# Performance work log

Hardware: AMD Instinct MI355X
Metric: run time of the kernel (lower is better)

## Reference

```python
import jax, jax.numpy as jnp
import numpy as np

N_NODES = 50000
N_EDGES = 800000
HIDDEN = 128


def setup_inputs() -> dict:
    key = jax.random.key(0)
    k1, k2, k3, k4, k5, k6 = jax.random.split(key, 6)
    node_features = jax.random.normal(k1, (N_NODES, HIDDEN), dtype=jnp.float32)
    src = jax.random.randint(k2, (N_EDGES,), 0, N_NODES)
    tgt = jax.random.randint(k3, (N_EDGES,), 0, N_NODES)
    gcn_norm = jax.random.uniform(k4, (N_EDGES,), dtype=jnp.float32)
    scale = 1.0 / np.sqrt(HIDDEN)
    W1 = jax.random.normal(k5, (HIDDEN, HIDDEN), dtype=jnp.float32) * scale
    b1 = jnp.zeros((HIDDEN,), dtype=jnp.float32)
    W2 = jax.random.normal(k6, (HIDDEN, HIDDEN), dtype=jnp.float32) * scale
    b2 = jnp.zeros((HIDDEN,), dtype=jnp.float32)
    return {"node_features": node_features, "src": src, "tgt": tgt,
            "gcn_norm": gcn_norm, "W1": W1, "b1": b1, "W2": W2, "b2": b2}


def reference(node_features, src, tgt, gcn_norm, W1, b1, W2, b2):
    # broadcast source node states to edges: [E, H]
    edge_states = node_features[src]
    # edge Dense + activation, scaled by gcn normalization (dropout = identity at inference)
    messages = gcn_norm[:, None] * jax.nn.relu(edge_states @ W1 + b1)
    # scatter-sum messages to target nodes: [N, H]
    pooled = jax.ops.segment_sum(messages, tgt, num_segments=node_features.shape[0])
    # node Dense + activation, then residual add of target feature
    hidden = jax.nn.relu(pooled @ W2 + b2)
    return hidden + node_features
```

## Files before the change

### kernel.cpp

```cpp
#include <hip/hip_runtime.h>

#define H 128

typedef short short8 __attribute__((ext_vector_type(8)));
typedef float floatx4 __attribute__((ext_vector_type(4)));

__device__ __forceinline__ short f2bf(float f) {
  union { float f; unsigned u; } v; v.f = f;
  unsigned r = v.u + 0x7fffu + ((v.u >> 16) & 1u);
  return (short)(r >> 16);
}
__device__ __forceinline__ float bf2f(unsigned u16) {
  union { unsigned u; float f; } v; v.u = u16 << 16;
  return v.f;
}

__global__ __launch_bounds__(256) void pack_count(
    const float* __restrict__ W1, const float* __restrict__ W2,
    short* __restrict__ Bp1, short* __restrict__ Bp2,
    const int* __restrict__ tgt, int* __restrict__ counts,
    int* __restrict__ rank, int E) {
  if (blockIdx.x < 16) {
    const int t = blockIdx.x * 256 + threadIdx.x;
    const float* W = (t >> 11) ? W2 : W1;
    short* Bp = (t >> 11) ? Bp2 : Bp1;
    const int i = t & 2047;
    const int lane = i & 63, ks = (i >> 6) & 3, nt = i >> 8;
    const int n = nt * 16 + (lane & 15);
    const int k0 = ks * 32 + ((lane >> 4) << 3);
    short8 v;
#pragma unroll
    for (int j = 0; j < 8; j++) v[j] = f2bf(W[(k0 + j) * H + n]);
    *reinterpret_cast<short8*>(Bp + (size_t)i * 8) = v;
  } else {
    const int e = (blockIdx.x - 16) * 256 + threadIdx.x;
    if (e < E) rank[e] = atomicAdd(&counts[tgt[e]], 1);
  }
}

template <bool A_BF16, bool C_BF16, bool RESID>
__global__ __launch_bounds__(256) void gemm_mfma(
    const void* __restrict__ Av, const short* __restrict__ Bp,
    const float* __restrict__ bias, const float* __restrict__ R,
    void* __restrict__ Cv, int M) {
  __shared__ int4 bLds[2048];
  const int tid = threadIdx.x;
  {
    const int4* g = reinterpret_cast<const int4*>(Bp);
#pragma unroll
    for (int i = 0; i < 8; i++) bLds[tid + i * 256] = g[tid + i * 256];
  }
  __syncthreads();

  const int wv = tid >> 6;
  const int lane = tid & 63;
  const int m0 = blockIdx.x * 64 + wv * 16;

  floatx4 acc[8];
#pragma unroll
  for (int nt = 0; nt < 8; nt++) acc[nt] = (floatx4)0.f;

  const int arow = lane & 15;
  const int kb = (lane >> 4) << 3;
  const short8* bL = reinterpret_cast<const short8*>(bLds);

#pragma unroll
  for (int ks = 0; ks < 4; ks++) {
    short8 af;
    {
      int row = min(m0 + arow, M - 1);
      const size_t off = (size_t)row * H + (ks << 5) + kb;
      if (A_BF16) {
        af = *reinterpret_cast<const short8*>((const short*)Av + off);
      } else {
        const float* ap = (const float*)Av + off;
        floatx4 x0 = *reinterpret_cast<const floatx4*>(ap);
        floatx4 x1 = *reinterpret_cast<const floatx4*>(ap + 4);
        af[0] = f2bf(x0[0]); af[1] = f2bf(x0[1]);
        af[2] = f2bf(x0[2]); af[3] = f2bf(x0[3]);
        af[4] = f2bf(x1[0]); af[5] = f2bf(x1[1]);
        af[6] = f2bf(x1[2]); af[7] = f2bf(x1[3]);
      }
    }
#pragma unroll
    for (int nt = 0; nt < 8; nt++) {
      const short8 bf = bL[((nt << 2) | ks) * 64 + lane];
      acc[nt] = __builtin_amdgcn_mfma_f32_16x16x32_bf16(af, bf, acc[nt], 0, 0, 0);
    }
  }

  const int crow = (lane >> 4) << 2;
  const int ccol = lane & 15;
#pragma unroll
  for (int nt = 0; nt < 8; nt++) {
    const int col = (nt << 4) + ccol;
    const float bv = bias[col];
#pragma unroll
    for (int r = 0; r < 4; r++) {
      const int row = m0 + crow + r;
      if (row < M) {
        float v = fmaxf(acc[nt][r] + bv, 0.f);
        if (RESID) v += R[(size_t)row * H + col];
        if (C_BF16)
          ((short*)Cv)[(size_t)row * H + col] = f2bf(v);
        else
          ((float*)Cv)[(size_t)row * H + col] = v;
      }
    }
  }
}


__global__ __launch_bounds__(256) void scan_partial(
    const int* __restrict__ counts, int* __restrict__ blockSums, int N) {
  const int tid = threadIdx.x;
  const int base = blockIdx.x * 1024 + tid * 4;
  int4 v = make_int4(0, 0, 0, 0);
  if (base + 3 < N) {
    v = *reinterpret_cast<const int4*>(counts + base);
  } else if (base < N) {
    const int n = N - base;
    v.x = counts[base];
    if (n > 1) v.y = counts[base + 1];
    if (n > 2) v.z = counts[base + 2];
  }
  int s = v.x + v.y + v.z + v.w;
#pragma unroll
  for (int d = 1; d < 64; d <<= 1) s += __shfl_xor(s, d);
  __shared__ int ws[4];
  if ((tid & 63) == 0) ws[tid >> 6] = s;
  __syncthreads();
  if (tid == 0) blockSums[blockIdx.x] = ws[0] + ws[1] + ws[2] + ws[3];
}

__global__ __launch_bounds__(256) void scan_final(
    const int* __restrict__ counts, const int* __restrict__ blockSums,
    int* __restrict__ offsets, int N, int E, int nb) {
  __shared__ int sPrefix;
  const int tid = threadIdx.x, lane = tid & 63, wv = tid >> 6;
  if (tid < 64) {
    const int v = (tid < nb) ? blockSums[tid] : 0;
    int x = v;
#pragma unroll
    for (int d = 1; d < 64; d <<= 1) {
      int t = __shfl_up(x, d);
      if (lane >= d) x += t;
    }
    if (tid == blockIdx.x) sPrefix = x - v;
  }

  const int base = blockIdx.x * 1024 + tid * 4;
  int4 v = make_int4(0, 0, 0, 0);
  if (base + 3 < N) {
    v = *reinterpret_cast<const int4*>(counts + base);
  } else if (base < N) {
    const int n = N - base;
    v.x = counts[base];
    if (n > 1) v.y = counts[base + 1];
    if (n > 2) v.z = counts[base + 2];
  }
  const int s = v.x + v.y + v.z + v.w;
  int x = s;
#pragma unroll
  for (int d = 1; d < 64; d <<= 1) {
    int t = __shfl_up(x, d);
    if (lane >= d) x += t;
  }
  __shared__ int ws[4];
  if (lane == 63) ws[wv] = x;
  __syncthreads();
  int wbase = 0;
  for (int i = 0; i < wv; i++) wbase += ws[i];

  const int excl = sPrefix + wbase + (x - s);
  const int o0 = excl, o1 = o0 + v.x, o2 = o1 + v.y, o3 = o2 + v.z;
  if (base + 3 < N) {
    *reinterpret_cast<int4*>(offsets + base) = make_int4(o0, o1, o2, o3);
  } else if (base < N) {
    const int n = N - base;
    offsets[base] = o0;
    if (n > 1) offsets[base + 1] = o1;
    if (n > 2) offsets[base + 2] = o2;
  }
  if (blockIdx.x == 0 && tid == 0) offsets[N] = E;
}

__global__ __launch_bounds__(256) void fill_edges(
    const int* __restrict__ src, const int* __restrict__ tgt,
    const float* __restrict__ norm, const int* __restrict__ offsets,
    const int* __restrict__ rank, unsigned* __restrict__ pairs, int E) {
  int e = blockIdx.x * blockDim.x + threadIdx.x;
  if (e >= E) return;
  const int pos = offsets[tgt[e]] + rank[e];
  pairs[pos] = (unsigned)(unsigned short)src[e] |
               ((unsigned)(unsigned short)f2bf(norm[e]) << 16);
}

__global__ __launch_bounds__(256) void pull_pool(
    const unsigned short* __restrict__ Y, const unsigned* __restrict__ pairs,
    const int* __restrict__ offsets, unsigned* __restrict__ pooled, int N) {
  const int node = blockIdx.x * 4 + (threadIdx.x >> 6);
  if (node >= N) return;
  const int lane = threadIdx.x & 63;
  int i = offsets[node];
  const int iend = offsets[node + 1];

  float ax = 0.f, ay = 0.f;
  for (; i + 7 < iend; i += 8) {
    const uint4 q0 = *reinterpret_cast<const uint4*>(pairs + i);
    const uint4 q1 = *reinterpret_cast<const uint4*>(pairs + i + 4);
    const unsigned p[8] = {q0.x, q0.y, q0.z, q0.w, q1.x, q1.y, q1.z, q1.w};
    unsigned v[8];
#pragma unroll
    for (int j = 0; j < 8; j++)
      v[j] = *reinterpret_cast<const unsigned*>(
          Y + (size_t)(p[j] & 0xffffu) * H + lane * 2);
#pragma unroll
    for (int j = 0; j < 8; j++) {
      const float n = bf2f(p[j] >> 16);
      ax = fmaf(n, bf2f(v[j] & 0xffffu), ax);
      ay = fmaf(n, bf2f(v[j] >> 16), ay);
    }
  }
  for (; i < iend; i++) {
    const unsigned p = pairs[i];
    const unsigned v = *reinterpret_cast<const unsigned*>(
        Y + (size_t)(p & 0xffffu) * H + lane * 2);
    const float n = bf2f(p >> 16);
    ax = fmaf(n, bf2f(v & 0xffffu), ax);
    ay = fmaf(n, bf2f(v >> 16), ay);
  }
  pooled[(size_t)node * 64 + lane] =
      ((unsigned)(unsigned short)f2bf(ay) << 16) | (unsigned short)f2bf(ax);
}

extern "C" void kernel_launch(void* const* d_in, const int* in_sizes, int n_in,
                              void* d_out, int out_size, void* d_ws, size_t ws_size,
                              hipStream_t stream) {
  const float* X    = (const float*)d_in[0];
  const int*   src  = (const int*)d_in[1];
  const int*   tgt  = (const int*)d_in[2];
  const float* norm = (const float*)d_in[3];
  const float* W1   = (const float*)d_in[4];
  const float* b1   = (const float*)d_in[5];
  const float* W2   = (const float*)d_in[6];
  const float* b2   = (const float*)d_in[7];
  float* out = (float*)d_out;

  const int N = in_sizes[0] / H;
  const int E = in_sizes[1];

  auto align_up = [](size_t x) { return (x + 255) & ~(size_t)255; };
  char* w = (char*)d_ws;
  unsigned short* Ybf   = (unsigned short*)w; w += align_up((size_t)N * H * 2);
  unsigned short* pool  = (unsigned short*)w; w += align_up((size_t)N * H * 2);
  int*   counts   = (int*)w;   w += align_up((size_t)N * sizeof(int));
  int*   offsets  = (int*)w;   w += align_up((size_t)(N + 1) * sizeof(int));
  int*   rank     = (int*)w;   w += align_up((size_t)E * sizeof(int));
  int*   blockSums= (int*)w;   w += align_up((size_t)1024 * sizeof(int));
  short* Bp1      = (short*)w; w += align_up((size_t)16384 * sizeof(short));
  short* Bp2      = (short*)w; w += align_up((size_t)16384 * sizeof(short));
  unsigned* pairs = (unsigned*)w; w += align_up((size_t)E * sizeof(unsigned));

  hipMemsetAsync(counts, 0, (size_t)N * sizeof(int), stream);

  const int eb = (E + 255) / 256;
  pack_count<<<eb + 16, 256, 0, stream>>>(W1, W2, Bp1, Bp2, tgt, counts, rank, E);

  const int gemm_blocks = (N + 63) / 64;
  gemm_mfma<false, true, false><<<gemm_blocks, 256, 0, stream>>>(
      X, Bp1, b1, nullptr, Ybf, N);

  const int nb = (N + 1023) / 1024;
  scan_partial<<<nb, 256, 0, stream>>>(counts, blockSums, N);
  scan_final<<<nb, 256, 0, stream>>>(counts, blockSums, offsets, N, E, nb);

  fill_edges<<<eb, 256, 0, stream>>>(src, tgt, norm, offsets, rank, pairs, E);

  pull_pool<<<(N + 3) / 4, 256, 0, stream>>>(
      Ybf, pairs, offsets, (unsigned*)pool, N);

  gemm_mfma<true, false, true><<<gemm_blocks, 256, 0, stream>>>(
      pool, Bp2, b2, X, out, N);
}
```

Measured before the change: 209.5 us.

## Fuse pull-pool with second GEMM and merge count with first GEMM

```diff
diff --git a/kernel.cpp b/kernel.cpp
--- a/kernel.cpp
+++ b/kernel.cpp
@@ -15,46 +15,31 @@
   return v.f;
 }
 
-__global__ __launch_bounds__(256) void pack_count(
-    const float* __restrict__ W1, const float* __restrict__ W2,
-    short* __restrict__ Bp1, short* __restrict__ Bp2,
-    const int* __restrict__ tgt, int* __restrict__ counts,
-    int* __restrict__ rank, int E) {
-  if (blockIdx.x < 16) {
-    const int t = blockIdx.x * 256 + threadIdx.x;
-    const float* W = (t >> 11) ? W2 : W1;
-    short* Bp = (t >> 11) ? Bp2 : Bp1;
-    const int i = t & 2047;
+template <int NTHREADS>
+__device__ __forceinline__ void pack_W_lds(const float* __restrict__ W,
+                                           short8* bLds, int tid) {
+#pragma unroll
+  for (int i = tid; i < 2048; i += NTHREADS) {
     const int lane = i & 63, ks = (i >> 6) & 3, nt = i >> 8;
     const int n = nt * 16 + (lane & 15);
     const int k0 = ks * 32 + ((lane >> 4) << 3);
     short8 v;
 #pragma unroll
     for (int j = 0; j < 8; j++) v[j] = f2bf(W[(k0 + j) * H + n]);
-    *reinterpret_cast<short8*>(Bp + (size_t)i * 8) = v;
-  } else {
-    const int e = (blockIdx.x - 16) * 256 + threadIdx.x;
-    if (e < E) rank[e] = atomicAdd(&counts[tgt[e]], 1);
-  }
-}
-
-template <bool A_BF16, bool C_BF16, bool RESID>
-__global__ __launch_bounds__(256) void gemm_mfma(
-    const void* __restrict__ Av, const short* __restrict__ Bp,
-    const float* __restrict__ bias, const float* __restrict__ R,
-    void* __restrict__ Cv, int M) {
-  __shared__ int4 bLds[2048];
-  const int tid = threadIdx.x;
-  {
-    const int4* g = reinterpret_cast<const int4*>(Bp);
-#pragma unroll
-    for (int i = 0; i < 8; i++) bLds[tid + i * 256] = g[tid + i * 256];
-  }
+    bLds[i] = v;
+  }
+}
+
+__device__ void gemm1_dev(int bid, int tid, const float* __restrict__ A,
+                          const float* __restrict__ W1,
+                          const float* __restrict__ bias,
+                          unsigned short* __restrict__ C, int M,
+                          short8* bLds) {
+  pack_W_lds<256>(W1, bLds, tid);
   __syncthreads();
 
-  const int wv = tid >> 6;
-  const int lane = tid & 63;
-  const int m0 = blockIdx.x * 64 + wv * 16;
+  const int wv = tid >> 6, lane = tid & 63;
+  const int m0 = bid * 64 + wv * 16;
 
   floatx4 acc[8];
 #pragma unroll
@@ -62,31 +47,23 @@
 
   const int arow = lane & 15;
   const int kb = (lane >> 4) << 3;
-  const short8* bL = reinterpret_cast<const short8*>(bLds);
 
 #pragma unroll
   for (int ks = 0; ks < 4; ks++) {
     short8 af;
     {
       int row = min(m0 + arow, M - 1);
-      const size_t off = (size_t)row * H + (ks << 5) + kb;
-      if (A_BF16) {
-        af = *reinterpret_cast<const short8*>((const short*)Av + off);
-      } else {
-        const float* ap = (const float*)Av + off;
-        floatx4 x0 = *reinterpret_cast<const floatx4*>(ap);
-        floatx4 x1 = *reinterpret_cast<const floatx4*>(ap + 4);
-        af[0] = f2bf(x0[0]); af[1] = f2bf(x0[1]);
-        af[2] = f2bf(x0[2]); af[3] = f2bf(x0[3]);
-        af[4] = f2bf(x1[0]); af[5] = f2bf(x1[1]);
-        af[6] = f2bf(x1[2]); af[7] = f2bf(x1[3]);
-      }
-    }
-#pragma unroll
-    for (int nt = 0; nt < 8; nt++) {
-      const short8 bf = bL[((nt << 2) | ks) * 64 + lane];
-      acc[nt] = __builtin_amdgcn_mfma_f32_16x16x32_bf16(af, bf, acc[nt], 0, 0, 0);
-    }
+      const float* ap = A + (size_t)row * H + (ks << 5) + kb;
+      floatx4 x0 = *reinterpret_cast<const floatx4*>(ap);
+      floatx4 x1 = *reinterpret_cast<const floatx4*>(ap + 4);
+      af[0] = f2bf(x0[0]); af[1] = f2bf(x0[1]);
+      af[2] = f2bf(x0[2]); af[3] = f2bf(x0[3]);
+      af[4] = f2bf(x1[0]); af[5] = f2bf(x1[1]);
+      af[6] = f2bf(x1[2]); af[7] = f2bf(x1[3]);
+    }
+#pragma unroll
+    for (int nt = 0; nt < 8; nt++)
+      acc[nt] = __builtin_amdgcn_mfma_f32_16x16x32_bf16(af, bLds[((nt << 2) | ks) * 64 + lane], acc[nt], 0, 0, 0);
   }
 
   const int crow = (lane >> 4) << 2;
@@ -100,13 +77,24 @@
       const int row = m0 + crow + r;
       if (row < M) {
         float v = fmaxf(acc[nt][r] + bv, 0.f);
-        if (RESID) v += R[(size_t)row * H + col];
-        if (C_BF16)
-          ((short*)Cv)[(size_t)row * H + col] = f2bf(v);
-        else
-          ((float*)Cv)[(size_t)row * H + col] = v;
+        C[(size_t)row * H + col] = (unsigned short)f2bf(v);
       }
     }
+  }
+}
+
+__global__ __launch_bounds__(256) void k1_count_gemm1(
+    const int* __restrict__ tgt, int* __restrict__ counts,
+    int* __restrict__ rank, int E,
+    const float* __restrict__ X, const float* __restrict__ W1,
+    const float* __restrict__ b1, unsigned short* __restrict__ Ybf,
+    int N, int nCnt) {
+  __shared__ short8 bLds[2048];
+  if ((int)blockIdx.x < nCnt) {
+    const int e = blockIdx.x * 256 + threadIdx.x;
+    if (e < E) rank[e] = atomicAdd(&counts[tgt[e]], 1);
+  } else {
+    gemm1_dev(blockIdx.x - nCnt, threadIdx.x, X, W1, b1, Ybf, N, bLds);
   }
 }
 
@@ -196,42 +184,86 @@
                ((unsigned)(unsigned short)f2bf(norm[e]) << 16);
 }
 
-__global__ __launch_bounds__(256) void pull_pool(
+__global__ __launch_bounds__(512) void k5_pull_gemm2(
     const unsigned short* __restrict__ Y, const unsigned* __restrict__ pairs,
-    const int* __restrict__ offsets, unsigned* __restrict__ pooled, int N) {
-  const int node = blockIdx.x * 4 + (threadIdx.x >> 6);
-  if (node >= N) return;
-  const int lane = threadIdx.x & 63;
-  int i = offsets[node];
-  const int iend = offsets[node + 1];
-
-  float ax = 0.f, ay = 0.f;
-  for (; i + 7 < iend; i += 8) {
-    const uint4 q0 = *reinterpret_cast<const uint4*>(pairs + i);
-    const uint4 q1 = *reinterpret_cast<const uint4*>(pairs + i + 4);
-    const unsigned p[8] = {q0.x, q0.y, q0.z, q0.w, q1.x, q1.y, q1.z, q1.w};
-    unsigned v[8];
-#pragma unroll
-    for (int j = 0; j < 8; j++)
-      v[j] = *reinterpret_cast<const unsigned*>(
-          Y + (size_t)(p[j] & 0xffffu) * H + lane * 2);
-#pragma unroll
-    for (int j = 0; j < 8; j++) {
-      const float n = bf2f(p[j] >> 16);
-      ax = fmaf(n, bf2f(v[j] & 0xffffu), ax);
-      ay = fmaf(n, bf2f(v[j] >> 16), ay);
-    }
-  }
-  for (; i < iend; i++) {
-    const unsigned p = pairs[i];
-    const unsigned v = *reinterpret_cast<const unsigned*>(
-        Y + (size_t)(p & 0xffffu) * H + lane * 2);
-    const float n = bf2f(p >> 16);
-    ax = fmaf(n, bf2f(v & 0xffffu), ax);
-    ay = fmaf(n, bf2f(v >> 16), ay);
-  }
-  pooled[(size_t)node * 64 + lane] =
-      ((unsigned)(unsigned short)f2bf(ay) << 16) | (unsigned short)f2bf(ax);
+    const int* __restrict__ offsets, const float* __restrict__ W2,
+    const float* __restrict__ b2, const float* __restrict__ X,
+    float* __restrict__ out, int N) {
+  __shared__ short8 bLds[2048];
+  __shared__ unsigned short aLds[128][136];
+  const int tid = threadIdx.x, wv = tid >> 6, lane = tid & 63;
+
+  pack_W_lds<512>(W2, bLds, tid);
+
+  const int rowBase = blockIdx.x * 128 + wv * 16;
+#pragma unroll 1
+  for (int r = 0; r < 16; r++) {
+    const int node = rowBase + r;
+    float ax = 0.f, ay = 0.f;
+    if (node < N) {
+      int i = offsets[node];
+      const int iend = offsets[node + 1];
+      for (; i + 7 < iend; i += 8) {
+        const uint4 q0 = *reinterpret_cast<const uint4*>(pairs + i);
+        const uint4 q1 = *reinterpret_cast<const uint4*>(pairs + i + 4);
+        const unsigned p[8] = {q0.x, q0.y, q0.z, q0.w, q1.x, q1.y, q1.z, q1.w};
+        unsigned v[8];
+#pragma unroll
+        for (int j = 0; j < 8; j++)
+          v[j] = *reinterpret_cast<const unsigned*>(
+              Y + (size_t)(p[j] & 0xffffu) * H + lane * 2);
+#pragma unroll
+        for (int j = 0; j < 8; j++) {
+          const float n = bf2f(p[j] >> 16);
+          ax = fmaf(n, bf2f(v[j] & 0xffffu), ax);
+          ay = fmaf(n, bf2f(v[j] >> 16), ay);
+        }
+      }
+      for (; i < iend; i++) {
+        const unsigned p = pairs[i];
+        const unsigned v = *reinterpret_cast<const unsigned*>(
+            Y + (size_t)(p & 0xffffu) * H + lane * 2);
+        const float n = bf2f(p >> 16);
+        ax = fmaf(n, bf2f(v & 0xffffu), ax);
+        ay = fmaf(n, bf2f(v >> 16), ay);
+      }
+    }
+    *reinterpret_cast<unsigned*>(&aLds[wv * 16 + r][lane * 2]) =
+        ((unsigned)(unsigned short)f2bf(ay) << 16) | (unsigned short)f2bf(ax);
+  }
+  __syncthreads();
+
+  floatx4 acc[8];
+#pragma unroll
+  for (int nt = 0; nt < 8; nt++) acc[nt] = (floatx4)0.f;
+
+  const int arow = lane & 15;
+  const int kb = (lane >> 4) << 3;
+
+#pragma unroll
+  for (int ks = 0; ks < 4; ks++) {
+    const short8 af = *reinterpret_cast<const short8*>(
+        &aLds[wv * 16 + arow][(ks << 5) + kb]);
+#pragma unroll
+    for (int nt = 0; nt < 8; nt++)
+      acc[nt] = __builtin_amdgcn_mfma_f32_16x16x32_bf16(af, bLds[((nt << 2) | ks) * 64 + lane], acc[nt], 0, 0, 0);
+  }
+
+  const int crow = (lane >> 4) << 2;
+  const int ccol = lane & 15;
+#pragma unroll
+  for (int nt = 0; nt < 8; nt++) {
+    const int col = (nt << 4) + ccol;
+    const float bv = b2[col];
+#pragma unroll
+    for (int r = 0; r < 4; r++) {
+      const int row = rowBase + crow + r;
+      if (row < N) {
+        const float v = fmaxf(acc[nt][r] + bv, 0.f);
+        out[(size_t)row * H + col] = v + X[(size_t)row * H + col];
+      }
+    }
+  }
 }
 
 extern "C" void kernel_launch(void* const* d_in, const int* in_sizes, int n_in,
@@ -253,23 +285,18 @@
   auto align_up = [](size_t x) { return (x + 255) & ~(size_t)255; };
   char* w = (char*)d_ws;
   unsigned short* Ybf   = (unsigned short*)w; w += align_up((size_t)N * H * 2);
-  unsigned short* pool  = (unsigned short*)w; w += align_up((size_t)N * H * 2);
   int*   counts   = (int*)w;   w += align_up((size_t)N * sizeof(int));
   int*   offsets  = (int*)w;   w += align_up((size_t)(N + 1) * sizeof(int));
   int*   rank     = (int*)w;   w += align_up((size_t)E * sizeof(int));
   int*   blockSums= (int*)w;   w += align_up((size_t)1024 * sizeof(int));
-  short* Bp1      = (short*)w; w += align_up((size_t)16384 * sizeof(short));
-  short* Bp2      = (short*)w; w += align_up((size_t)16384 * sizeof(short));
   unsigned* pairs = (unsigned*)w; w += align_up((size_t)E * sizeof(unsigned));
 
   hipMemsetAsync(counts, 0, (size_t)N * sizeof(int), stream);
 
   const int eb = (E + 255) / 256;
-  pack_count<<<eb + 16, 256, 0, stream>>>(W1, W2, Bp1, Bp2, tgt, counts, rank, E);
-
   const int gemm_blocks = (N + 63) / 64;
-  gemm_mfma<false, true, false><<<gemm_blocks, 256, 0, stream>>>(
-      X, Bp1, b1, nullptr, Ybf, N);
+  k1_count_gemm1<<<eb + gemm_blocks, 256, 0, stream>>>(
+      tgt, counts, rank, E, X, W1, b1, Ybf, N, eb);
 
   const int nb = (N + 1023) / 1024;
   scan_partial<<<nb, 256, 0, stream>>>(counts, blockSums, N);
@@ -277,9 +304,6 @@
 
   fill_edges<<<eb, 256, 0, stream>>>(src, tgt, norm, offsets, rank, pairs, E);
 
-  pull_pool<<<(N + 3) / 4, 256, 0, stream>>>(
-      Ybf, pairs, offsets, (unsigned*)pool, N);
-
-  gemm_mfma<true, false, true><<<gemm_blocks, 256, 0, stream>>>(
-      pool, Bp2, b2, X, out, N);
-}
+  k5_pull_gemm2<<<(N + 127) / 128, 512, 0, stream>>>(
+      Ybf, pairs, offsets, W2, b2, X, out, N);
+}
```

New measurement: 234.4 us. 1.12x slower.

## Fuse edge counting into first GEMM launch and vectorize pull tail loop

Applied to the files above, without the earlier changes.

```diff
diff --git a/kernel.cpp b/kernel.cpp
--- a/kernel.cpp
+++ b/kernel.cpp
@@ -15,36 +15,27 @@
   return v.f;
 }
 
-__global__ __launch_bounds__(256) void pack_count(
+__global__ __launch_bounds__(256) void pack_W(
     const float* __restrict__ W1, const float* __restrict__ W2,
-    short* __restrict__ Bp1, short* __restrict__ Bp2,
-    const int* __restrict__ tgt, int* __restrict__ counts,
-    int* __restrict__ rank, int E) {
-  if (blockIdx.x < 16) {
-    const int t = blockIdx.x * 256 + threadIdx.x;
-    const float* W = (t >> 11) ? W2 : W1;
-    short* Bp = (t >> 11) ? Bp2 : Bp1;
-    const int i = t & 2047;
-    const int lane = i & 63, ks = (i >> 6) & 3, nt = i >> 8;
-    const int n = nt * 16 + (lane & 15);
-    const int k0 = ks * 32 + ((lane >> 4) << 3);
-    short8 v;
-#pragma unroll
-    for (int j = 0; j < 8; j++) v[j] = f2bf(W[(k0 + j) * H + n]);
-    *reinterpret_cast<short8*>(Bp + (size_t)i * 8) = v;
-  } else {
-    const int e = (blockIdx.x - 16) * 256 + threadIdx.x;
-    if (e < E) rank[e] = atomicAdd(&counts[tgt[e]], 1);
-  }
+    short* __restrict__ Bp1, short* __restrict__ Bp2) {
+  const int t = blockIdx.x * 256 + threadIdx.x;
+  const float* W = (t >> 11) ? W2 : W1;
+  short* Bp = (t >> 11) ? Bp2 : Bp1;
+  const int i = t & 2047;
+  const int lane = i & 63, ks = (i >> 6) & 3, nt = i >> 8;
+  const int n = nt * 16 + (lane & 15);
+  const int k0 = ks * 32 + ((lane >> 4) << 3);
+  short8 v;
+#pragma unroll
+  for (int j = 0; j < 8; j++) v[j] = f2bf(W[(k0 + j) * H + n]);
+  *reinterpret_cast<short8*>(Bp + (size_t)i * 8) = v;
 }
 
 template <bool A_BF16, bool C_BF16, bool RESID>
-__global__ __launch_bounds__(256) void gemm_mfma(
-    const void* __restrict__ Av, const short* __restrict__ Bp,
+__device__ __forceinline__ void gemm_dev(
+    int bid, int tid, const void* __restrict__ Av, const short* __restrict__ Bp,
     const float* __restrict__ bias, const float* __restrict__ R,
-    void* __restrict__ Cv, int M) {
-  __shared__ int4 bLds[2048];
-  const int tid = threadIdx.x;
+    void* __restrict__ Cv, int M, int4* bLds) {
   {
     const int4* g = reinterpret_cast<const int4*>(Bp);
 #pragma unroll
@@ -52,9 +43,8 @@
   }
   __syncthreads();
 
-  const int wv = tid >> 6;
-  const int lane = tid & 63;
-  const int m0 = blockIdx.x * 64 + wv * 16;
+  const int wv = tid >> 6, lane = tid & 63;
+  const int m0 = bid * 64 + wv * 16;
 
   floatx4 acc[8];
 #pragma unroll
@@ -83,10 +73,9 @@
       }
     }
 #pragma unroll
-    for (int nt = 0; nt < 8; nt++) {
-      const short8 bf = bL[((nt << 2) | ks) * 64 + lane];
-      acc[nt] = __builtin_amdgcn_mfma_f32_16x16x32_bf16(af, bf, acc[nt], 0, 0, 0);
-    }
+    for (int nt = 0; nt < 8; nt++)
+      acc[nt] = __builtin_amdgcn_mfma_f32_16x16x32_bf16(
+          af, bL[((nt << 2) | ks) * 64 + lane], acc[nt], 0, 0, 0);
   }
 
   const int crow = (lane >> 4) << 2;
@@ -108,6 +97,31 @@
       }
     }
   }
+}
+
+__global__ __launch_bounds__(256) void k1_count_gemm1(
+    const int* __restrict__ tgt, int* __restrict__ counts,
+    int* __restrict__ rank, int E,
+    const float* __restrict__ X, const short* __restrict__ Bp1,
+    const float* __restrict__ b1, unsigned short* __restrict__ Ybf,
+    int N, int nCnt) {
+  __shared__ int4 bLds[2048];
+  if ((int)blockIdx.x < nCnt) {
+    const int e = blockIdx.x * 256 + threadIdx.x;
+    if (e < E) rank[e] = atomicAdd(&counts[tgt[e]], 1);
+  } else {
+    gemm_dev<false, true, false>(blockIdx.x - nCnt, threadIdx.x, X, Bp1, b1,
+                                 nullptr, Ybf, N, bLds);
+  }
+}
+
+__global__ __launch_bounds__(256) void gemm2_kernel(
+    const unsigned short* __restrict__ pool, const short* __restrict__ Bp2,
+    const float* __restrict__ b2, const float* __restrict__ X,
+    float* __restrict__ out, int N) {
+  __shared__ int4 bLds[2048];
+  gemm_dev<true, false, true>(blockIdx.x, threadIdx.x, pool, Bp2, b2, X, out,
+                              N, bLds);
 }
 
 
@@ -222,13 +236,21 @@
       ay = fmaf(n, bf2f(v[j] >> 16), ay);
     }
   }
-  for (; i < iend; i++) {
-    const unsigned p = pairs[i];
-    const unsigned v = *reinterpret_cast<const unsigned*>(
-        Y + (size_t)(p & 0xffffu) * H + lane * 2);
-    const float n = bf2f(p >> 16);
-    ax = fmaf(n, bf2f(v & 0xffffu), ax);
-    ay = fmaf(n, bf2f(v >> 16), ay);
+  if (i < iend) {
+    unsigned p[8];
+#pragma unroll
+    for (int j = 0; j < 8; j++) p[j] = (i + j < iend) ? pairs[i + j] : 0u;
+    unsigned v[8];
+#pragma unroll
+    for (int j = 0; j < 8; j++)
+      v[j] = *reinterpret_cast<const unsigned*>(
+          Y + (size_t)(p[j] & 0xffffu) * H + lane * 2);
+#pragma unroll
+    for (int j = 0; j < 8; j++) {
+      const float n = bf2f(p[j] >> 16);
+      ax = fmaf(n, bf2f(v[j] & 0xffffu), ax);
+      ay = fmaf(n, bf2f(v[j] >> 16), ay);
+    }
   }
   pooled[(size_t)node * 64 + lane] =
       ((unsigned)(unsigned short)f2bf(ay) << 16) | (unsigned short)f2bf(ax);
@@ -264,12 +286,12 @@
 
   hipMemsetAsync(counts, 0, (size_t)N * sizeof(int), stream);
 
+  pack_W<<<16, 256, 0, stream>>>(W1, W2, Bp1, Bp2);
+
   const int eb = (E + 255) / 256;
-  pack_count<<<eb + 16, 256, 0, stream>>>(W1, W2, Bp1, Bp2, tgt, counts, rank, E);
-
   const int gemm_blocks = (N + 63) / 64;
-  gemm_mfma<false, true, false><<<gemm_blocks, 256, 0, stream>>>(
-      X, Bp1, b1, nullptr, Ybf, N);
+  k1_count_gemm1<<<eb + gemm_blocks, 256, 0, stream>>>(
+      tgt, counts, rank, E, X, Bp1, b1, Ybf, N, eb);
 
   const int nb = (N + 1023) / 1024;
   scan_partial<<<nb, 256, 0, stream>>>(counts, blockSums, N);
@@ -280,6 +302,5 @@
   pull_pool<<<(N + 3) / 4, 256, 0, stream>>>(
       Ybf, pairs, offsets, (unsigned*)pool, N);
 
-  gemm_mfma<true, false, true><<<gemm_blocks, 256, 0, stream>>>(
-      pool, Bp2, b2, X, out, N);
-}
+  gemm2_kernel<<<gemm_blocks, 256, 0, stream>>>(pool, Bp2, b2, X, out, N);
+}
```

Result: faster. 199.6 us (-4.7%).
